# Performance work log

Measured on AMD Instinct MI355X. Metric: run time of the kernel, lower is better.

## Reference

```python
import jax, jax.numpy as jnp
import numpy as np

K_DIM = 64  # contraction dim for scores; scale = 1/sqrt(K_DIM)


def setup_inputs() -> dict:
    key = jax.random.key(0)
    ks = jax.random.split(key, 8)
    B, T, L, D, H, E, V = 128, 16, 32, 256, 8, 64, 64
    return {
        "queries": jax.random.normal(ks[0], (B, T, L, D), dtype=jnp.float32),
        "keys": jax.random.normal(ks[1], (B, T, L, D), dtype=jnp.float32),
        "values": jax.random.normal(ks[2], (B, T, L, D), dtype=jnp.float32),
        "attn_mask": jax.random.uniform(ks[3], (B, B), dtype=jnp.float32),
        "Wq": jax.random.normal(ks[4], (D, H, E), dtype=jnp.float32) * 0.05,
        "Wk": jax.random.normal(ks[5], (D, H, E), dtype=jnp.float32) * 0.05,
        "Wv": jax.random.normal(ks[6], (D, H, V), dtype=jnp.float32) * 0.05,
        "w_head": jax.random.normal(ks[7], (H,), dtype=jnp.float32),
    }


def reference(queries, keys, values, attn_mask, Wq, Wk, Wv, w_head):
    # QKV projections (EinsumDense 'abcd,def->abcef', no bias): [b,t,l,h,e]
    Q = jnp.einsum('btld,dhe->btlhe', queries, Wq)
    K = jnp.einsum('btld,dhe->btlhe', keys, Wk)
    V = jnp.einsum('btld,dhe->btlhe', values, Wv)

    scale = 1.0 / jnp.sqrt(jnp.float32(K_DIM))
    # cross-batch attention scores: [t, l, h, B, b]
    scores = jnp.einsum('Btlhe,btlhe->tlhBb', Q, K) * scale
    # multiplicative mask, broadcast over trailing [B, b]
    scores = scores * attn_mask
    # Dropout is identity at inference (Keras Dropout, training=False)

    attn = jnp.einsum('tlhBb,btlhe->Bthle', jax.nn.softmax(scores, axis=-1), V)
    # head-mixing output ('bthle,h->btle'): [b, t, l, v_dim]
    attn_output = jnp.einsum('bthle,h->btle', attn, w_head)
    return (attn_output, scores)
```

## Files before the change

### kernel.cpp

```cpp
#include <hip/hip_runtime.h>
#include <hip/hip_bf16.h>


using bf16x8 = __attribute__((ext_vector_type(8))) __bf16;
using bf16x4 = __attribute__((ext_vector_type(4))) __bf16;
using f32x4  = __attribute__((ext_vector_type(4))) float;

__device__ __forceinline__ f32x4 mfma16(bf16x8 a, bf16x8 b, f32x4 c) {
  return __builtin_amdgcn_mfma_f32_16x16x32_bf16(a, b, c, 0, 0, 0);
}

__global__ __launch_bounds__(512) void k0_wt(const float* __restrict__ Wq,
                                             const float* __restrict__ Wk,
                                             const float* __restrict__ Wv,
                                             __bf16* __restrict__ Wt) {
  int f   = blockIdx.x * 512 + threadIdx.x;
  int mat = f >> 14;
  int rem = f & 16383;
  int d8  = rem >> 9;
  int col = rem & 511;
  const float* W = (mat == 0) ? Wq : (mat == 1) ? Wk : Wv;
  bf16x8 v;
#pragma unroll
  for (int i = 0; i < 8; ++i) v[i] = (__bf16)W[(d8 * 8 + i) * 512 + col];
  *(bf16x8*)(Wt + mat * 131072 + col * 256 + d8 * 8) = v;
}

__global__ __launch_bounds__(512, 4) void k1_proj(const float* __restrict__ xq,
                                                  const float* __restrict__ xk,
                                                  const float* __restrict__ xv,
                                                  const __bf16* __restrict__ Wt,
                                                  __bf16* __restrict__ qkv) {
  __shared__ char smem[65536];
  const int tid  = threadIdx.x;
  const int tl   = blockIdx.x;
  const int m    = blockIdx.y;
  const int lane = tid & 63, w = tid >> 6;
  const int lrow = lane & 15, lk = lane >> 4;
  const f32x4 z4 = {0.f, 0.f, 0.f, 0.f};

  const float* xm = (m == 0) ? xq : (m == 1) ? xk : xv;

#pragma unroll
  for (int i = 0; i < 8; ++i) {
    int c = i * 512 + tid;
    int row = c >> 5, sl = c & 31;
    const float* g = xm + (size_t)row * 131072 + (size_t)tl * 256 + sl * 8;
    float4 f0 = *(const float4*)g;
    float4 f1 = *(const float4*)(g + 4);
    bf16x8 v;
    v[0] = (__bf16)f0.x; v[1] = (__bf16)f0.y; v[2] = (__bf16)f0.z; v[3] = (__bf16)f0.w;
    v[4] = (__bf16)f1.x; v[5] = (__bf16)f1.y; v[6] = (__bf16)f1.z; v[7] = (__bf16)f1.w;
    *(bf16x8*)(smem + row * 512 + ((sl ^ (row & 7)) << 4)) = v;
  }
  __syncthreads();

  const int h = w;
  const __bf16* wbase = Wt + (size_t)(m * 512 + h * 64) * 256;
  __bf16* dst = qkv + (size_t)(tl * 8 + h) * 32768 + m * 8192;

#pragma unroll 1
  for (int eq = 0; eq < 4; ++eq) {
    const __bf16* wrow = wbase + (eq * 16 + lrow) * 256 + lk * 8;
    bf16x8 wreg[8];
#pragma unroll
    for (int kk = 0; kk < 8; ++kk) wreg[kk] = *(const bf16x8*)(wrow + kk * 32);

#pragma unroll 1
    for (int bh = 0; bh < 2; ++bh) {
      f32x4 acc[4];
#pragma unroll
      for (int bi = 0; bi < 4; ++bi) acc[bi] = z4;

#pragma unroll
      for (int kk = 0; kk < 8; ++kk) {
        bf16x8 xf[4];
#pragma unroll
        for (int bi = 0; bi < 4; ++bi) {
          int row = bh * 64 + bi * 16 + lrow;
          xf[bi] = *(const bf16x8*)(smem + row * 512 +
                                    ((kk * 64 + lk * 16) ^ ((row & 7) << 4)));
        }
        if (m < 2) {
#pragma unroll
          for (int bi = 0; bi < 4; ++bi) acc[bi] = mfma16(wreg[kk], xf[bi], acc[bi]);
        } else {
#pragma unroll
          for (int bi = 0; bi < 4; ++bi) acc[bi] = mfma16(xf[bi], wreg[kk], acc[bi]);
        }
      }

      if (m < 2) {
#pragma unroll
        for (int bi = 0; bi < 4; ++bi) {
          bf16x4 v;
#pragma unroll
          for (int r = 0; r < 4; ++r) v[r] = (__bf16)acc[bi][r];
          int b = bh * 64 + bi * 16 + lrow;
          *(bf16x4*)(dst + b * 64 + eq * 16 + lk * 4) = v;
        }
      } else {
#pragma unroll
        for (int bi = 0; bi < 4; ++bi) {
          bf16x4 v;
#pragma unroll
          for (int r = 0; r < 4; ++r) v[r] = (__bf16)acc[bi][r];
          int e = eq * 16 + lrow;
          *(bf16x4*)(dst + e * 128 + bh * 64 + bi * 16 + lk * 4) = v;
        }
      }
    }
  }
}

__global__ __launch_bounds__(512) void k2_attn(const float* __restrict__ mask,
                                               const float* __restrict__ w_head,
                                               float* out_base) {
  __shared__ char smem[65536];
  const int tid  = threadIdx.x;
  const int tl   = blockIdx.x;
  const int lane = tid & 63, w = tid >> 6;
  const int lrow = lane & 15, lk = lane >> 4;
  const f32x4 z4 = {0.f, 0.f, 0.f, 0.f};

  float* scores = out_base + 4194304;

  float mreg[8][4];
#pragma unroll
  for (int ct = 0; ct < 8; ++ct)
#pragma unroll
    for (int r = 0; r < 4; ++r)
      mreg[ct][r] = mask[(w * 16 + lk * 4 + r) * 128 + ct * 16 + lrow];

  f32x4 oacc[4];
#pragma unroll
  for (int i = 0; i < 4; ++i) oacc[i] = z4;

  const int arow = w * 16 + lrow;

  for (int h = 0; h < 8; ++h) {
    const __bf16* slot = (const __bf16*)scores + (size_t)(tl * 8 + h) * 32768;
    float wh = w_head[h];

    bf16x8 a0 = *(const bf16x8*)(slot + arow * 64 + lk * 8);
    bf16x8 a1 = *(const bf16x8*)(slot + arow * 64 + 32 + lk * 8);

    __syncthreads();
#pragma unroll
    for (int i = 0; i < 2; ++i) {
      int cc = i * 512 + tid;
      int krow = cc >> 3, ks = cc & 7;
      uint4 kv = *(const uint4*)(slot + 8192 + krow * 64 + ks * 8);
      *(uint4*)(smem + krow * 128 + ((ks ^ (krow & 7)) << 4)) = kv;
      int e = cc >> 4, vs = cc & 15;
      uint4 vv = *(const uint4*)(slot + 16384 + e * 128 + vs * 8);
      *(uint4*)(smem + 16384 + e * 256 + ((vs ^ (e & 7)) << 4)) = vv;
    }
    __syncthreads();

    f32x4 sacc[8];
#pragma unroll
    for (int ct = 0; ct < 8; ++ct) {
      int bcol = ct * 16 + lrow;
      const char* kb = smem + bcol * 128;
      int bswz = (bcol & 7) << 4;
      bf16x8 b0 = *(const bf16x8*)(kb + ((lk * 16 + 0) ^ bswz));
      bf16x8 b1 = *(const bf16x8*)(kb + ((lk * 16 + 64) ^ bswz));
      sacc[ct] = mfma16(a0, b0, z4);
      sacc[ct] = mfma16(a1, b1, sacc[ct]);
    }

    float* srow = scores + (size_t)(tl * 8 + h) * 16384;
#pragma unroll
    for (int ct = 0; ct < 8; ++ct)
#pragma unroll
      for (int r = 0; r < 4; ++r) {
        float s = sacc[ct][r] * 0.125f * mreg[ct][r];
        sacc[ct][r] = s;
        srow[(w * 16 + lk * 4 + r) * 128 + ct * 16 + lrow] = s;
      }

#pragma unroll
    for (int r = 0; r < 4; ++r) {
      float mx = sacc[0][r];
#pragma unroll
      for (int ct = 1; ct < 8; ++ct) mx = fmaxf(mx, sacc[ct][r]);
      mx = fmaxf(mx, __shfl_xor(mx, 1));
      mx = fmaxf(mx, __shfl_xor(mx, 2));
      mx = fmaxf(mx, __shfl_xor(mx, 4));
      mx = fmaxf(mx, __shfl_xor(mx, 8));
      float sum = 0.f;
#pragma unroll
      for (int ct = 0; ct < 8; ++ct) {
        float p = __expf(sacc[ct][r] - mx);
        sacc[ct][r] = p;
        sum += p;
      }
      sum += __shfl_xor(sum, 1);
      sum += __shfl_xor(sum, 2);
      sum += __shfl_xor(sum, 4);
      sum += __shfl_xor(sum, 8);
      float fct = wh / sum;
      int row16 = lk * 4 + r;
      char* pb = smem + 32768 + w * 4096 + row16 * 256;
      int pswz = (row16 & 7) << 4;
#pragma unroll
      for (int ct = 0; ct < 8; ++ct) {
        int col = ct * 16 + lrow;
        *(__bf16*)(pb + ((col * 2) ^ pswz)) = (__bf16)(sacc[ct][r] * fct);
      }
    }

    const char* pab = smem + 32768 + w * 4096 + lrow * 256;
    int paswz = (lrow & 7) << 4;
    bf16x8 pa[4];
#pragma unroll
    for (int kk = 0; kk < 4; ++kk)
      pa[kk] = *(const bf16x8*)(pab + ((lk * 16 + kk * 64) ^ paswz));
#pragma unroll
    for (int ct2 = 0; ct2 < 4; ++ct2) {
      int ecol = ct2 * 16 + lrow;
      const char* vb = smem + 16384 + ecol * 256;
      int vswz = (ecol & 7) << 4;
#pragma unroll
      for (int kk = 0; kk < 4; ++kk) {
        bf16x8 b = *(const bf16x8*)(vb + ((lk * 16 + kk * 64) ^ vswz));
        oacc[ct2] = mfma16(pa[kk], b, oacc[ct2]);
      }
    }
  }

#pragma unroll
  for (int ct2 = 0; ct2 < 4; ++ct2)
#pragma unroll
    for (int r = 0; r < 4; ++r) {
      int brow = w * 16 + lk * 4 + r;
      int e    = ct2 * 16 + lrow;
      out_base[(size_t)(brow * 512 + tl) * 64 + e] = oacc[ct2][r];
    }
}

extern "C" void kernel_launch(void* const* d_in, const int* in_sizes, int n_in,
                              void* d_out, int out_size, void* d_ws, size_t ws_size,
                              hipStream_t stream) {
  const float* q    = (const float*)d_in[0];
  const float* k    = (const float*)d_in[1];
  const float* v    = (const float*)d_in[2];
  const float* mask = (const float*)d_in[3];
  const float* Wq   = (const float*)d_in[4];
  const float* Wk   = (const float*)d_in[5];
  const float* Wv   = (const float*)d_in[6];
  const float* wh   = (const float*)d_in[7];
  float* out = (float*)d_out;

  __bf16* Wt  = (__bf16*)out;
  __bf16* qkv = (__bf16*)(out + 4194304);

  hipLaunchKernelGGL(k0_wt,   dim3(96),      dim3(512), 0, stream, Wq, Wk, Wv, Wt);
  hipLaunchKernelGGL(k1_proj, dim3(512, 3),  dim3(512), 0, stream, q, k, v, Wt, qkv);
  hipLaunchKernelGGL(k2_attn, dim3(512),     dim3(512), 0, stream, mask, wh, out);
}
```

Measured before the change: 263.4 us.

## Split projection blocks over head halves and compute full per-wave tiles

The projection kernel now launches 256-thread blocks over a (tl, head-half, matrix) grid, so each block covers four heads instead of eight. Each wave computes the full 128x64 output tile with 32 accumulators, loading weight fragments per k-step rather than per e-quarter. The input tile is loaded and converted twice as often, once per head half. The aim is more blocks for parallelism and more MFMA work per LDS read, at the cost of higher register pressure and duplicated input loads.

```diff
diff --git a/kernel.cpp b/kernel.cpp
--- a/kernel.cpp
+++ b/kernel.cpp
@@ -26,7 +26,7 @@
   *(bf16x8*)(Wt + mat * 131072 + col * 256 + d8 * 8) = v;
 }
 
-__global__ __launch_bounds__(512, 4) void k1_proj(const float* __restrict__ xq,
+__global__ __launch_bounds__(256, 2) void k1_proj(const float* __restrict__ xq,
                                                   const float* __restrict__ xk,
                                                   const float* __restrict__ xv,
                                                   const __bf16* __restrict__ Wt,
@@ -34,7 +34,8 @@
   __shared__ char smem[65536];
   const int tid  = threadIdx.x;
   const int tl   = blockIdx.x;
-  const int m    = blockIdx.y;
+  const int hh   = blockIdx.y;
+  const int m    = blockIdx.z;
   const int lane = tid & 63, w = tid >> 6;
   const int lrow = lane & 15, lk = lane >> 4;
   const f32x4 z4 = {0.f, 0.f, 0.f, 0.f};
@@ -42,8 +43,8 @@
   const float* xm = (m == 0) ? xq : (m == 1) ? xk : xv;
 
 #pragma unroll
-  for (int i = 0; i < 8; ++i) {
-    int c = i * 512 + tid;
+  for (int i = 0; i < 16; ++i) {
+    int c = i * 256 + tid;
     int row = c >> 5, sl = c & 31;
     const float* g = xm + (size_t)row * 131072 + (size_t)tl * 256 + sl * 8;
     float4 f0 = *(const float4*)g;
@@ -55,61 +56,76 @@
   }
   __syncthreads();
 
-  const int h = w;
+  const int h = hh * 4 + w;
   const __bf16* wbase = Wt + (size_t)(m * 512 + h * 64) * 256;
   __bf16* dst = qkv + (size_t)(tl * 8 + h) * 32768 + m * 8192;
 
-#pragma unroll 1
-  for (int eq = 0; eq < 4; ++eq) {
-    const __bf16* wrow = wbase + (eq * 16 + lrow) * 256 + lk * 8;
-    bf16x8 wreg[8];
-#pragma unroll
-    for (int kk = 0; kk < 8; ++kk) wreg[kk] = *(const bf16x8*)(wrow + kk * 32);
-
-#pragma unroll 1
-    for (int bh = 0; bh < 2; ++bh) {
-      f32x4 acc[4];
-#pragma unroll
-      for (int bi = 0; bi < 4; ++bi) acc[bi] = z4;
-
-#pragma unroll
-      for (int kk = 0; kk < 8; ++kk) {
-        bf16x8 xf[4];
-#pragma unroll
-        for (int bi = 0; bi < 4; ++bi) {
-          int row = bh * 64 + bi * 16 + lrow;
-          xf[bi] = *(const bf16x8*)(smem + row * 512 +
-                                    ((kk * 64 + lk * 16) ^ ((row & 7) << 4)));
-        }
-        if (m < 2) {
-#pragma unroll
-          for (int bi = 0; bi < 4; ++bi) acc[bi] = mfma16(wreg[kk], xf[bi], acc[bi]);
-        } else {
-#pragma unroll
-          for (int bi = 0; bi < 4; ++bi) acc[bi] = mfma16(xf[bi], wreg[kk], acc[bi]);
-        }
-      }
-
-      if (m < 2) {
-#pragma unroll
-        for (int bi = 0; bi < 4; ++bi) {
-          bf16x4 v;
-#pragma unroll
-          for (int r = 0; r < 4; ++r) v[r] = (__bf16)acc[bi][r];
-          int b = bh * 64 + bi * 16 + lrow;
-          *(bf16x4*)(dst + b * 64 + eq * 16 + lk * 4) = v;
-        }
-      } else {
-#pragma unroll
-        for (int bi = 0; bi < 4; ++bi) {
-          bf16x4 v;
-#pragma unroll
-          for (int r = 0; r < 4; ++r) v[r] = (__bf16)acc[bi][r];
-          int e = eq * 16 + lrow;
-          *(bf16x4*)(dst + e * 128 + bh * 64 + bi * 16 + lk * 4) = v;
-        }
-      }
-    }
+  f32x4 acc[8][4];
+#pragma unroll
+  for (int bi = 0; bi < 8; ++bi)
+#pragma unroll
+    for (int ci = 0; ci < 4; ++ci) acc[bi][ci] = z4;
+
+  if (m < 2) {
+#pragma unroll
+    for (int kk = 0; kk < 8; ++kk) {
+      bf16x8 wf[4];
+#pragma unroll
+      for (int ci = 0; ci < 4; ++ci)
+        wf[ci] = *(const bf16x8*)(wbase + (ci * 16 + lrow) * 256 + kk * 32 + lk * 8);
+      bf16x8 xf[8];
+#pragma unroll
+      for (int bi = 0; bi < 8; ++bi) {
+        int row = bi * 16 + lrow;
+        xf[bi] = *(const bf16x8*)(smem + row * 512 +
+                                  ((kk * 64 + lk * 16) ^ ((row & 7) << 4)));
+      }
+#pragma unroll
+      for (int bi = 0; bi < 8; ++bi)
+#pragma unroll
+        for (int ci = 0; ci < 4; ++ci)
+          acc[bi][ci] = mfma16(wf[ci], xf[bi], acc[bi][ci]);
+    }
+#pragma unroll
+    for (int bi = 0; bi < 8; ++bi)
+#pragma unroll
+      for (int ci = 0; ci < 4; ++ci) {
+        bf16x4 v;
+#pragma unroll
+        for (int r = 0; r < 4; ++r) v[r] = (__bf16)acc[bi][ci][r];
+        int b = bi * 16 + lrow;
+        *(bf16x4*)(dst + b * 64 + ci * 16 + lk * 4) = v;
+      }
+  } else {
+#pragma unroll
+    for (int kk = 0; kk < 8; ++kk) {
+      bf16x8 wf[4];
+#pragma unroll
+      for (int ci = 0; ci < 4; ++ci)
+        wf[ci] = *(const bf16x8*)(wbase + (ci * 16 + lrow) * 256 + kk * 32 + lk * 8);
+      bf16x8 xf[8];
+#pragma unroll
+      for (int bi = 0; bi < 8; ++bi) {
+        int row = bi * 16 + lrow;
+        xf[bi] = *(const bf16x8*)(smem + row * 512 +
+                                  ((kk * 64 + lk * 16) ^ ((row & 7) << 4)));
+      }
+#pragma unroll
+      for (int bi = 0; bi < 8; ++bi)
+#pragma unroll
+        for (int ci = 0; ci < 4; ++ci)
+          acc[bi][ci] = mfma16(xf[bi], wf[ci], acc[bi][ci]);
+    }
+#pragma unroll
+    for (int bi = 0; bi < 8; ++bi)
+#pragma unroll
+      for (int ci = 0; ci < 4; ++ci) {
+        bf16x4 v;
+#pragma unroll
+        for (int r = 0; r < 4; ++r) v[r] = (__bf16)acc[bi][ci][r];
+        int e = ci * 16 + lrow;
+        *(bf16x4*)(dst + e * 128 + bi * 16 + lk * 4) = v;
+      }
   }
 }
 
@@ -256,7 +272,7 @@
   __bf16* Wt  = (__bf16*)out;
   __bf16* qkv = (__bf16*)(out + 4194304);
 
-  hipLaunchKernelGGL(k0_wt,   dim3(96),      dim3(512), 0, stream, Wq, Wk, Wv, Wt);
-  hipLaunchKernelGGL(k1_proj, dim3(512, 3),  dim3(512), 0, stream, q, k, v, Wt, qkv);
-  hipLaunchKernelGGL(k2_attn, dim3(512),     dim3(512), 0, stream, mask, wh, out);
-}
+  hipLaunchKernelGGL(k0_wt,   dim3(96),        dim3(512), 0, stream, Wq, Wk, Wv, Wt);
+  hipLaunchKernelGGL(k1_proj, dim3(512, 2, 3), dim3(256), 0, stream, q, k, v, Wt, qkv);
+  hipLaunchKernelGGL(k2_attn, dim3(512),       dim3(512), 0, stream, mask, wh, out);
+}
```

New measurement: 279.6 us. 1.06x slower.
